# Optimization experiments

Hardware: AMD Instinct MI355X
Metric: run time of the kernel (lower is better)

## Reference

```python
import jax, jax.numpy as jnp
from jax import lax
import numpy as np

N = 200000
H = 64          # h
C = 2 * H       # 2h feature channels
L = 128         # voxel grid side
KV = 125        # 5^3 kernel volume
KEEP = KV // 2 + 1  # 63 offsets kept by mask type 'B' (incl. center)


def _build_kernel_map(coords):
    # coords: [N,3] int voxel coords, unique. Returns nidx [KEEP, N] int32, -1 if no neighbor.
    keys = (coords[:, 0].astype(np.int64) * L + coords[:, 1]) * L + coords[:, 2]
    order = np.argsort(keys)
    skeys = keys[order]
    nidx = np.full((KEEP, N), -1, dtype=np.int32)
    for k in range(KEEP):
        dx, dy, dz = k // 25 - 2, (k // 5) % 5 - 2, k % 5 - 2
        nc = coords + np.array([dx, dy, dz])
        inb = np.all((nc >= 0) & (nc < L), axis=1)
        qk = (nc[:, 0].astype(np.int64) * L + nc[:, 1]) * L + nc[:, 2]
        pos = np.searchsorted(skeys, qk)
        posc = np.minimum(pos, N - 1)
        found = inb & (skeys[posc] == qk)
        nidx[k] = np.where(found, order[posc].astype(np.int32), -1)
    return nidx


def setup_inputs() -> dict:
    key = jax.random.key(0)
    k1, k2, k3, k4, k5 = jax.random.split(key, 5)
    rng = np.random.default_rng(0)
    flat = rng.choice(L ** 3, size=N, replace=False)
    coords = np.stack(np.unravel_index(flat, (L, L, L)), axis=1).astype(np.int32)
    nidx = jnp.asarray(_build_kernel_map(coords))
    s = 0.05
    return {
        "x_feats": jax.random.normal(k1, (N, C), jnp.float32),
        "y_feats": jax.random.normal(k2, (N, C), jnp.float32),
        "Wa": jax.random.normal(k3, (C, H), jnp.float32) * s,
        "Wb": jax.random.normal(k4, (KV, H, H), jnp.float32) * s,
        "Wc": jax.random.normal(k5, (H, C), jnp.float32) * s,
        "nidx": nidx,
    }


def reference(x_feats, y_feats, Wa, Wb, Wc, nidx):
    # mask type 'B': zero kernel offsets >= KV//2 + 1
    mask = (jnp.arange(KV) < KEEP)[:, None, None].astype(Wb.dtype)
    Wb_kept = (Wb * mask)[:KEEP]  # [KEEP, H, H]; remaining offsets contribute 0

    def block(f):
        f = jax.nn.elu(f)
        f = f @ Wa                      # 1x1 conv 2h->h
        f = jax.nn.elu(f)
        # masked sparse 5^3 conv: gather-GEMM-accumulate over kernel offsets
        def body(acc, kw):
            idx, W = kw                 # idx [N], W [H,H]
            g = jnp.where((idx >= 0)[:, None], f[jnp.maximum(idx, 0)], 0.0)
            return acc + g @ W, None
        acc0 = jnp.zeros((f.shape[0], H), f.dtype)
        f, _ = lax.scan(body, acc0, (nidx, Wb_kept))
        f = jax.nn.elu(f)
        return f @ Wc                   # 1x1 conv h->2h

    out = x_feats + y_feats
    return x_feats + block(out)
```

## Files before the change

kernel.cpp:

```cpp
#include <hip/hip_runtime.h>
#include <cmath>

#define N_PTS 200000
#define HD 64
#define CD 128
#define KEEP 63

typedef __bf16 bf16;
typedef __bf16 bf16x4 __attribute__((ext_vector_type(4)));
typedef __bf16 bf16x8 __attribute__((ext_vector_type(8)));
typedef float f32x4 __attribute__((ext_vector_type(4)));
typedef float f32x16 __attribute__((ext_vector_type(16)));

__device__ __forceinline__ float elu_f(float v) {
    return v > 0.f ? v : __expf(v) - 1.f;
}

__global__ __launch_bounds__(256) void k_prep(const float* __restrict__ Wb,
                                              const float* __restrict__ Wc,
                                              const float* __restrict__ Wa,
                                              bf16* __restrict__ WbT,
                                              bf16* __restrict__ WcT2,
                                              bf16* __restrict__ WaT,
                                              bf16* __restrict__ zp) {
    int idx = blockIdx.x * 256 + threadIdx.x;
    if (idx < KEEP * HD * HD) {
        int k = idx >> 12;
        int rem = idx & 4095;
        int o = rem >> 6, i = rem & 63;
        int dst = ((i >> 4) * 2 + (o >> 5)) * 512 +
                  (((i >> 3) & 1) * 32 + (o & 31)) * 8 + (i & 7);
        WbT[(k << 12) + dst] = (bf16)Wb[(k * HD + i) * HD + o];
        return;
    }
    int e = idx - KEEP * HD * HD;
    if (e < CD * HD) {
        int c = e >> 6, h = e & 63;
        int dst = ((c >> 5) * 4 + (h >> 4)) * 512 +
                  ((((h >> 3) & 1) * 32) + (c & 31)) * 8 + (h & 7);
        WcT2[dst] = (bf16)Wc[h * CD + c];
        return;
    }
    e -= CD * HD;
    if (e < HD * CD) {
        int o = e >> 7, c = e & 127;
        int dst = ((c >> 4) * 2 + (o >> 5)) * 512 +
                  (((c >> 3) & 1) * 32 + (o & 31)) * 8 + (c & 7);
        WaT[dst] = (bf16)Wa[c * HD + o];
        return;
    }
    e -= HD * CD;
    if (e < 64) zp[e] = (bf16)0.f;
}

__global__ __launch_bounds__(256, 4) void k_stage1(const float* __restrict__ x,
                                                   const float* __restrict__ y,
                                                   const bf16* __restrict__ WaT,
                                                   bf16* __restrict__ f) {
    __shared__ bf16 pbuf[4][32 * 64];
    int tid = threadIdx.x;
    int wave = tid >> 6;
    int lane = tid & 63;
    int l31 = lane & 31;
    int half = lane >> 5;
    int pbase_w = blockIdx.x * 128 + wave * 32;
    int p = pbase_w + l31;
    int pc = p < N_PTS ? p : N_PTS - 1;

    const float* xr = x + (size_t)pc * CD;
    const float* yr = y + (size_t)pc * CD;

    f32x16 acc[2];
#pragma unroll
    for (int mt = 0; mt < 2; mt++)
#pragma unroll
        for (int r = 0; r < 16; r++) acc[mt][r] = 0.f;

    f32x4 xa[2], xb[2], ya[2], yb[2];
    {
        int c0 = half * 8;
        xa[0] = *(const f32x4*)(xr + c0);
        xb[0] = *(const f32x4*)(xr + c0 + 4);
        ya[0] = *(const f32x4*)(yr + c0);
        yb[0] = *(const f32x4*)(yr + c0 + 4);
    }
#pragma unroll
    for (int ks = 0; ks < 8; ks++) {
        int cur = ks & 1, nxt = cur ^ 1;
        bf16x8 a0 = *(const bf16x8*)(WaT + (ks * 2 + 0) * 512 + lane * 8);
        bf16x8 a1 = *(const bf16x8*)(WaT + (ks * 2 + 1) * 512 + lane * 8);
        __builtin_amdgcn_sched_barrier(0);
        if (ks < 7) {
            int c0 = half * 8 + (ks + 1) * 16;
            xa[nxt] = *(const f32x4*)(xr + c0);
            xb[nxt] = *(const f32x4*)(xr + c0 + 4);
            ya[nxt] = *(const f32x4*)(yr + c0);
            yb[nxt] = *(const f32x4*)(yr + c0 + 4);
        }
        bf16x8 bv;
#pragma unroll
        for (int jj = 0; jj < 4; jj++) {
            bv[jj]     = (bf16)elu_f(xa[cur][jj] + ya[cur][jj]);
            bv[4 + jj] = (bf16)elu_f(xb[cur][jj] + yb[cur][jj]);
        }
        acc[0] = __builtin_amdgcn_mfma_f32_32x32x16_bf16(a0, bv, acc[0], 0, 0, 0);
        acc[1] = __builtin_amdgcn_mfma_f32_32x32x16_bf16(a1, bv, acc[1], 0, 0, 0);
        __builtin_amdgcn_sched_barrier(0);
    }

    bf16* pb = pbuf[wave];
#pragma unroll
    for (int mt = 0; mt < 2; mt++) {
#pragma unroll
        for (int q = 0; q < 4; q++) {
            bf16x4 v;
#pragma unroll
            for (int jj = 0; jj < 4; jj++)
                v[jj] = (bf16)elu_f(acc[mt][q * 4 + jj]);
            int chunk = mt * 4 + q;
            *(bf16x4*)&pb[l31 * 64 + ((chunk ^ (l31 & 7)) * 8) + 4 * half] = v;
        }
    }
#pragma unroll
    for (int qq = 0; qq < 4; qq++) {
        int t = lane + 64 * qq;
        int row = t >> 3, ch = t & 7;
        int pos = ch ^ (row & 7);
        bf16x8 v = *(const bf16x8*)&pb[row * 64 + pos * 8];
        int pp = pbase_w + row;
        if (pp < N_PTS)
            *(bf16x8*)(f + (size_t)pp * HD + ch * 8) = v;
    }
}

struct GR { bf16x8 v[4]; };

__global__ __launch_bounds__(256, 2) void k_conv(const bf16* __restrict__ f,
                                                 const int* __restrict__ nidx,
                                                 const bf16* __restrict__ WbT,
                                                 const bf16* __restrict__ WcT2,
                                                 const bf16* __restrict__ zp,
                                                 const float* __restrict__ x,
                                                 float* __restrict__ out) {
    __shared__ bf16 lds_a[2][4096];
    __shared__ bf16 bounce[4][32 * 64];

    int tid = threadIdx.x;
    int wave = tid >> 6;
    int lane = tid & 63;
    int l31 = lane & 31;
    int half = lane >> 5;
    int g8 = lane >> 3;
    int l7 = lane & 7;
    int pbase = blockIdx.x * 128 + wave * 32;

    bf16* pb = bounce[wave];

    f32x16 acc[2];
#pragma unroll
    for (int mt = 0; mt < 2; mt++)
#pragma unroll
        for (int r = 0; r < 16; r++) acc[mt][r] = 0.f;

    auto ldidx4 = [&](int k, int i) -> int {
        int pp = pbase + i * 8 + g8;
        return (k < KEEP && pp < N_PTS) ? nidx[(size_t)k * N_PTS + pp] : -1;
    };
    auto gaddr = [&](int iv) -> const bf16* {
        return iv >= 0 ? f + (size_t)iv * HD + l7 * 8 : zp + l7 * 8;
    };
    auto gather4 = [&](GR& g, const int (&iv)[4]) {
#pragma unroll
        for (int i = 0; i < 4; i++)
            g.v[i] = *(const bf16x8*)gaddr(iv[i]);
    };
    auto dswrite = [&](const GR& g) {
#pragma unroll
        for (int i = 0; i < 4; i++) {
            int pp = i * 8 + g8;
            *(bf16x8*)&pb[pp * 64 + ((l7 ^ g8) * 8)] = g.v[i];
        }
    };
    auto stageIssue = [&](int k, bf16x8& s0, bf16x8& s1) {
        const bf16* wk = WbT + ((size_t)k << 12) + wave * 1024 + lane * 8;
        s0 = *(const bf16x8*)(wk);
        s1 = *(const bf16x8*)(wk + 512);
    };
    auto stageWrite = [&](int kb, const bf16x8& s0, const bf16x8& s1) {
        bf16* d = &lds_a[kb][wave * 1024 + lane * 8];
        *(bf16x8*)(d) = s0;
        *(bf16x8*)(d + 512) = s1;
    };
    auto mfma8_lds = [&](int kb) {
        const bf16* A = lds_a[kb];
#pragma unroll
        for (int ks = 0; ks < 4; ks++) {
            int ci = ks * 2 + half;
            bf16x8 fb = *(const bf16x8*)&pb[l31 * 64 + ((ci ^ (l31 & 7)) * 8)];
            bf16x8 a0 = *(const bf16x8*)&A[(ks * 2 + 0) * 512 + lane * 8];
            bf16x8 a1 = *(const bf16x8*)&A[(ks * 2 + 1) * 512 + lane * 8];
            acc[0] = __builtin_amdgcn_mfma_f32_32x32x16_bf16(a0, fb, acc[0], 0, 0, 0);
            acc[1] = __builtin_amdgcn_mfma_f32_32x32x16_bf16(a1, fb, acc[1], 0, 0, 0);
        }
    };
    auto substep = [&](int k, GR& gfill, const GR& gwrite, int (&slot)[4]) {
        bf16x8 sA0, sA1;
        stageIssue(k + 1, sA0, sA1);
        __builtin_amdgcn_sched_barrier(0);
        gather4(gfill, slot);
#pragma unroll
        for (int i = 0; i < 4; i++) slot[i] = ldidx4(k + 6, i);
        __builtin_amdgcn_sched_barrier(0);
        mfma8_lds(k & 1);
        __builtin_amdgcn_sched_barrier(0);
        dswrite(gwrite);
        stageWrite((k + 1) & 1, sA0, sA1);
        asm volatile("s_waitcnt lgkmcnt(0)" ::: "memory");
        __builtin_amdgcn_s_barrier();
        __builtin_amdgcn_sched_barrier(0);
    };

    int s0[4], s1[4], s2[4], s3[4];
#pragma unroll
    for (int i = 0; i < 4; i++) s0[i] = ldidx4(2, i);
#pragma unroll
    for (int i = 0; i < 4; i++) s1[i] = ldidx4(3, i);
#pragma unroll
    for (int i = 0; i < 4; i++) s2[i] = ldidx4(4, i);
#pragma unroll
    for (int i = 0; i < 4; i++) s3[i] = ldidx4(5, i);
    GR ge, go;
    {
        int i0[4], i1[4];
#pragma unroll
        for (int i = 0; i < 4; i++) i0[i] = ldidx4(0, i);
#pragma unroll
        for (int i = 0; i < 4; i++) i1[i] = ldidx4(1, i);
        GR g0;
        gather4(g0, i0);
        gather4(go, i1);
        bf16x8 sA0, sA1;
        stageIssue(0, sA0, sA1);
        dswrite(g0);
        stageWrite(0, sA0, sA1);
        asm volatile("s_waitcnt lgkmcnt(0)" ::: "memory");
        __builtin_amdgcn_s_barrier();
        __builtin_amdgcn_sched_barrier(0);
    }

    for (int j = 0; j < 15; j++) {
        int k = 4 * j;
        substep(k,     ge, go, s0);
        substep(k + 1, go, ge, s1);
        substep(k + 2, ge, go, s2);
        substep(k + 3, go, ge, s3);
    }
    substep(60, ge, go, s0);
    substep(61, go, ge, s1);
    mfma8_lds(0);

#pragma unroll
    for (int mt = 0; mt < 2; mt++) {
#pragma unroll
        for (int q = 0; q < 4; q++) {
            bf16x4 v;
#pragma unroll
            for (int jj = 0; jj < 4; jj++)
                v[jj] = (bf16)elu_f(acc[mt][q * 4 + jj]);
            int chunk = mt * 4 + q;
            *(bf16x4*)&pb[l31 * 64 + ((chunk ^ (l31 & 7)) * 8) + 4 * half] = v;
        }
    }
    bf16x8 pa[4];
#pragma unroll
    for (int ks = 0; ks < 4; ks++) {
        int ci = 2 * ks + half;
        pa[ks] = *(const bf16x8*)&pb[l31 * 64 + ((ci ^ (l31 & 7)) * 8)];
    }
#pragma unroll
    for (int ct = 0; ct < 4; ct++) {
        f32x16 o;
#pragma unroll
        for (int r = 0; r < 16; r++) o[r] = 0.f;
        int cc = ct * 32 + l31;
#pragma unroll
        for (int ks = 0; ks < 4; ks++) {
            bf16x8 bw = *(const bf16x8*)(WcT2 + ((ct * 4 + ks) << 9) + lane * 8);
            o = __builtin_amdgcn_mfma_f32_32x32x16_bf16(pa[ks], bw, o, 0, 0, 0);
        }
        int prow_base = pbase + 4 * half;
#pragma unroll
        for (int r = 0; r < 16; r++) {
            int prow = prow_base + (r & 3) + 8 * (r >> 2);
            if (prow < N_PTS) {
                size_t off = (size_t)prow * CD + cc;
                out[off] = x[off] + o[r];
            }
        }
    }
}

extern "C" void kernel_launch(void* const* d_in, const int* in_sizes, int n_in,
                              void* d_out, int out_size, void* d_ws, size_t ws_size,
                              hipStream_t stream) {
    const float* x  = (const float*)d_in[0];
    const float* y  = (const float*)d_in[1];
    const float* Wa = (const float*)d_in[2];
    const float* Wb = (const float*)d_in[3];
    const float* Wc = (const float*)d_in[4];
    const int* nidx = (const int*)d_in[5];
    float* out = (float*)d_out;

    char* ws = (char*)d_ws;
    bf16* f    = (bf16*)ws;
    bf16* WbT  = (bf16*)(ws + 25624576);
    bf16* WcT2 = (bf16*)(ws + 25624576 + 516096);
    bf16* WaT  = (bf16*)(ws + 25624576 + 516096 + 16384);
    bf16* zp   = (bf16*)(ws + 25624576 + 516096 + 16384 + 16384);

    k_prep<<<1073, 256, 0, stream>>>(Wb, Wc, Wa, WbT, WcT2, WaT, zp);
    k_stage1<<<1563, 256, 0, stream>>>(x, y, WaT, f);
    k_conv<<<1563, 256, 0, stream>>>(f, nidx, WbT, WcT2, zp, x, out);
}
```

Before: 501.7 us.

## Process 64 points per wave in sparse conv to reuse staged weights

Each wave of the conv kernel now handles 64 points instead of 32, keeping four accumulator tiles, so every kernel-offset weight tile loaded into LDS feeds twice as many MFMAs. The aim is to halve per-point weight staging and barrier overhead. The index prefetch depth drops from four offsets ahead to two to save registers. Register pressure roughly doubles for gather buffers and accumulators, which risks spills or lower occupancy, and the grid is halved to 782 blocks. The stage1 grid change to 1564 blocks looks incidental.

```diff
diff --git a/kernel.cpp b/kernel.cpp
--- a/kernel.cpp
+++ b/kernel.cpp
@@ -133,7 +133,7 @@
     }
 }
 
-struct GR { bf16x8 v[4]; };
+struct GR8 { bf16x8 v[8]; };
 
 __global__ __launch_bounds__(256, 2) void k_conv(const bf16* __restrict__ f,
                                                  const int* __restrict__ nidx,
@@ -143,7 +143,7 @@
                                                  const float* __restrict__ x,
                                                  float* __restrict__ out) {
     __shared__ bf16 lds_a[2][4096];
-    __shared__ bf16 bounce[4][32 * 64];
+    __shared__ bf16 bounce[4][64 * 64];
 
     int tid = threadIdx.x;
     int wave = tid >> 6;
@@ -152,33 +152,35 @@
     int half = lane >> 5;
     int g8 = lane >> 3;
     int l7 = lane & 7;
-    int pbase = blockIdx.x * 128 + wave * 32;
+    int pbase = blockIdx.x * 256 + wave * 64;
 
     bf16* pb = bounce[wave];
 
-    f32x16 acc[2];
-#pragma unroll
-    for (int mt = 0; mt < 2; mt++)
-#pragma unroll
-        for (int r = 0; r < 16; r++) acc[mt][r] = 0.f;
-
-    auto ldidx4 = [&](int k, int i) -> int {
+    f32x16 acc[2][2];
+#pragma unroll
+    for (int a = 0; a < 2; a++)
+#pragma unroll
+        for (int b = 0; b < 2; b++)
+#pragma unroll
+            for (int r = 0; r < 16; r++) acc[a][b][r] = 0.f;
+
+    auto ldidx8 = [&](int k, int i) -> int {
         int pp = pbase + i * 8 + g8;
         return (k < KEEP && pp < N_PTS) ? nidx[(size_t)k * N_PTS + pp] : -1;
     };
     auto gaddr = [&](int iv) -> const bf16* {
         return iv >= 0 ? f + (size_t)iv * HD + l7 * 8 : zp + l7 * 8;
     };
-    auto gather4 = [&](GR& g, const int (&iv)[4]) {
-#pragma unroll
-        for (int i = 0; i < 4; i++)
+    auto gather8 = [&](GR8& g, const int (&iv)[8]) {
+#pragma unroll
+        for (int i = 0; i < 8; i++)
             g.v[i] = *(const bf16x8*)gaddr(iv[i]);
     };
-    auto dswrite = [&](const GR& g) {
-#pragma unroll
-        for (int i = 0; i < 4; i++) {
-            int pp = i * 8 + g8;
-            *(bf16x8*)&pb[pp * 64 + ((l7 ^ g8) * 8)] = g.v[i];
+    auto dswrite8 = [&](const GR8& g) {
+#pragma unroll
+        for (int i = 0; i < 8; i++) {
+            int r = i * 8 + g8;
+            *(bf16x8*)&pb[r * 64 + ((l7 ^ g8) * 8)] = g.v[i];
         }
     };
     auto stageIssue = [&](int k, bf16x8& s0, bf16x8& s1) {
@@ -191,110 +193,108 @@
         *(bf16x8*)(d) = s0;
         *(bf16x8*)(d + 512) = s1;
     };
-    auto mfma8_lds = [&](int kb) {
+    auto mfma16 = [&](int kb) {
         const bf16* A = lds_a[kb];
 #pragma unroll
         for (int ks = 0; ks < 4; ks++) {
-            int ci = ks * 2 + half;
-            bf16x8 fb = *(const bf16x8*)&pb[l31 * 64 + ((ci ^ (l31 & 7)) * 8)];
             bf16x8 a0 = *(const bf16x8*)&A[(ks * 2 + 0) * 512 + lane * 8];
             bf16x8 a1 = *(const bf16x8*)&A[(ks * 2 + 1) * 512 + lane * 8];
-            acc[0] = __builtin_amdgcn_mfma_f32_32x32x16_bf16(a0, fb, acc[0], 0, 0, 0);
-            acc[1] = __builtin_amdgcn_mfma_f32_32x32x16_bf16(a1, fb, acc[1], 0, 0, 0);
-        }
-    };
-    auto substep = [&](int k, GR& gfill, const GR& gwrite, int (&slot)[4]) {
+            int ci = ks * 2 + half;
+#pragma unroll
+            for (int set = 0; set < 2; set++) {
+                int r = set * 32 + l31;
+                bf16x8 fb = *(const bf16x8*)&pb[r * 64 + ((ci ^ (l31 & 7)) * 8)];
+                acc[0][set] = __builtin_amdgcn_mfma_f32_32x32x16_bf16(a0, fb, acc[0][set], 0, 0, 0);
+                acc[1][set] = __builtin_amdgcn_mfma_f32_32x32x16_bf16(a1, fb, acc[1][set], 0, 0, 0);
+            }
+        }
+    };
+    auto substep = [&](int k, GR8& gfill, const GR8& gwrite, int (&slot)[8]) {
         bf16x8 sA0, sA1;
         stageIssue(k + 1, sA0, sA1);
         __builtin_amdgcn_sched_barrier(0);
-        gather4(gfill, slot);
-#pragma unroll
-        for (int i = 0; i < 4; i++) slot[i] = ldidx4(k + 6, i);
-        __builtin_amdgcn_sched_barrier(0);
-        mfma8_lds(k & 1);
-        __builtin_amdgcn_sched_barrier(0);
-        dswrite(gwrite);
+        gather8(gfill, slot);
+#pragma unroll
+        for (int i = 0; i < 8; i++) slot[i] = ldidx8(k + 4, i);
+        __builtin_amdgcn_sched_barrier(0);
+        mfma16(k & 1);
+        __builtin_amdgcn_sched_barrier(0);
+        dswrite8(gwrite);
         stageWrite((k + 1) & 1, sA0, sA1);
         asm volatile("s_waitcnt lgkmcnt(0)" ::: "memory");
         __builtin_amdgcn_s_barrier();
         __builtin_amdgcn_sched_barrier(0);
     };
 
-    int s0[4], s1[4], s2[4], s3[4];
-#pragma unroll
-    for (int i = 0; i < 4; i++) s0[i] = ldidx4(2, i);
-#pragma unroll
-    for (int i = 0; i < 4; i++) s1[i] = ldidx4(3, i);
-#pragma unroll
-    for (int i = 0; i < 4; i++) s2[i] = ldidx4(4, i);
-#pragma unroll
-    for (int i = 0; i < 4; i++) s3[i] = ldidx4(5, i);
-    GR ge, go;
+    int s0[8], s1[8];
+#pragma unroll
+    for (int i = 0; i < 8; i++) s0[i] = ldidx8(2, i);
+#pragma unroll
+    for (int i = 0; i < 8; i++) s1[i] = ldidx8(3, i);
+    GR8 ge, go;
     {
-        int i0[4], i1[4];
-#pragma unroll
-        for (int i = 0; i < 4; i++) i0[i] = ldidx4(0, i);
-#pragma unroll
-        for (int i = 0; i < 4; i++) i1[i] = ldidx4(1, i);
-        GR g0;
-        gather4(g0, i0);
-        gather4(go, i1);
+        int i0[8], i1[8];
+#pragma unroll
+        for (int i = 0; i < 8; i++) i0[i] = ldidx8(0, i);
+#pragma unroll
+        for (int i = 0; i < 8; i++) i1[i] = ldidx8(1, i);
+        GR8 g0;
+        gather8(g0, i0);
+        gather8(go, i1);
         bf16x8 sA0, sA1;
         stageIssue(0, sA0, sA1);
-        dswrite(g0);
+        dswrite8(g0);
         stageWrite(0, sA0, sA1);
         asm volatile("s_waitcnt lgkmcnt(0)" ::: "memory");
         __builtin_amdgcn_s_barrier();
         __builtin_amdgcn_sched_barrier(0);
     }
 
-    for (int j = 0; j < 15; j++) {
-        int k = 4 * j;
-        substep(k,     ge, go, s0);
-        substep(k + 1, go, ge, s1);
-        substep(k + 2, ge, go, s2);
-        substep(k + 3, go, ge, s3);
-    }
-    substep(60, ge, go, s0);
-    substep(61, go, ge, s1);
-    mfma8_lds(0);
-
-#pragma unroll
-    for (int mt = 0; mt < 2; mt++) {
-#pragma unroll
-        for (int q = 0; q < 4; q++) {
-            bf16x4 v;
-#pragma unroll
-            for (int jj = 0; jj < 4; jj++)
-                v[jj] = (bf16)elu_f(acc[mt][q * 4 + jj]);
-            int chunk = mt * 4 + q;
-            *(bf16x4*)&pb[l31 * 64 + ((chunk ^ (l31 & 7)) * 8) + 4 * half] = v;
-        }
-    }
-    bf16x8 pa[4];
-#pragma unroll
-    for (int ks = 0; ks < 4; ks++) {
-        int ci = 2 * ks + half;
-        pa[ks] = *(const bf16x8*)&pb[l31 * 64 + ((ci ^ (l31 & 7)) * 8)];
-    }
-#pragma unroll
-    for (int ct = 0; ct < 4; ct++) {
-        f32x16 o;
-#pragma unroll
-        for (int r = 0; r < 16; r++) o[r] = 0.f;
-        int cc = ct * 32 + l31;
+    for (int j = 0; j < 31; j++) {
+        substep(2 * j,     ge, go, s0);
+        substep(2 * j + 1, go, ge, s1);
+    }
+    mfma16(0);
+
+#pragma unroll
+    for (int pt = 0; pt < 2; pt++) {
+#pragma unroll
+        for (int mt = 0; mt < 2; mt++) {
+#pragma unroll
+            for (int q = 0; q < 4; q++) {
+                bf16x4 v;
+#pragma unroll
+                for (int jj = 0; jj < 4; jj++)
+                    v[jj] = (bf16)elu_f(acc[mt][pt][q * 4 + jj]);
+                int chunk = mt * 4 + q;
+                *(bf16x4*)&pb[l31 * 64 + ((chunk ^ (l31 & 7)) * 8) + 4 * half] = v;
+            }
+        }
+        bf16x8 pa[4];
 #pragma unroll
         for (int ks = 0; ks < 4; ks++) {
-            bf16x8 bw = *(const bf16x8*)(WcT2 + ((ct * 4 + ks) << 9) + lane * 8);
-            o = __builtin_amdgcn_mfma_f32_32x32x16_bf16(pa[ks], bw, o, 0, 0, 0);
-        }
-        int prow_base = pbase + 4 * half;
-#pragma unroll
-        for (int r = 0; r < 16; r++) {
-            int prow = prow_base + (r & 3) + 8 * (r >> 2);
-            if (prow < N_PTS) {
-                size_t off = (size_t)prow * CD + cc;
-                out[off] = x[off] + o[r];
+            int ci = 2 * ks + half;
+            pa[ks] = *(const bf16x8*)&pb[l31 * 64 + ((ci ^ (l31 & 7)) * 8)];
+        }
+#pragma unroll
+        for (int ct = 0; ct < 4; ct++) {
+            f32x16 o;
+#pragma unroll
+            for (int r = 0; r < 16; r++) o[r] = 0.f;
+            int cc = ct * 32 + l31;
+#pragma unroll
+            for (int ks = 0; ks < 4; ks++) {
+                bf16x8 bw = *(const bf16x8*)(WcT2 + ((ct * 4 + ks) << 9) + lane * 8);
+                o = __builtin_amdgcn_mfma_f32_32x32x16_bf16(pa[ks], bw, o, 0, 0, 0);
+            }
+            int prow_base = pbase + pt * 32 + 4 * half;
+#pragma unroll
+            for (int r = 0; r < 16; r++) {
+                int prow = prow_base + (r & 3) + 8 * (r >> 2);
+                if (prow < N_PTS) {
+                    size_t off = (size_t)prow * CD + cc;
+                    out[off] = x[off] + o[r];
+                }
             }
         }
     }
@@ -319,6 +319,6 @@
     bf16* zp   = (bf16*)(ws + 25624576 + 516096 + 16384 + 16384);
 
     k_prep<<<1073, 256, 0, stream>>>(Wb, Wc, Wa, WbT, WcT2, WaT, zp);
-    k_stage1<<<1563, 256, 0, stream>>>(x, y, WaT, f);
-    k_conv<<<1563, 256, 0, stream>>>(f, nidx, WbT, WcT2, zp, x, out);
-}
+    k_stage1<<<1564, 256, 0, stream>>>(x, y, WaT, f);
+    k_conv<<<782, 256, 0, stream>>>(f, nidx, WbT, WcT2, zp, x, out);
+}
```

Measured after the change: 558.5 us. 11.3% more time.
